# Kernel optimization log

Measured on AMD Instinct MI355X. Metric: run time of the kernel, lower is better.

The kernel has to match this reference:

```python
import jax, jax.numpy as jnp
import numpy as np

NODE_DIM = 128
EDGE_DIM = 128
N_RADIAL = 16
MAX_Z = 100
N_NODES = 50000
N_EDGES = 800000


def setup_inputs() -> dict:
    key = jax.random.key(0)
    ks = jax.random.split(key, 8)
    z = jax.random.randint(ks[0], (N_NODES,), 0, MAX_Z)
    rbf = jax.random.uniform(ks[1], (N_EDGES, N_RADIAL), dtype=jnp.float32)
    idx_i = jax.random.randint(ks[2], (N_EDGES,), 0, N_NODES)
    idx_j = jax.random.randint(ks[3], (N_EDGES,), 0, N_NODES)
    # learned parameters
    embed_table = jax.random.normal(ks[4], (MAX_Z, NODE_DIM), dtype=jnp.float32)
    rbf_w = jax.random.normal(ks[5], (N_RADIAL, EDGE_DIM), dtype=jnp.float32) * (1.0 / np.sqrt(N_RADIAL))
    in_dim = 2 * NODE_DIM + EDGE_DIM
    edge_w = jax.random.normal(ks[6], (in_dim, EDGE_DIM), dtype=jnp.float32) * (1.0 / np.sqrt(in_dim))
    edge_b = jnp.zeros((EDGE_DIM,), dtype=jnp.float32)
    return {"z": z, "rbf": rbf, "idx_i": idx_i, "idx_j": idx_j,
            "embed_table": embed_table, "rbf_w": rbf_w,
            "edge_w": edge_w, "edge_b": edge_b}


def reference(z, rbf, idx_i, idx_j, embed_table, rbf_w, edge_w, edge_b):
    # node embedding lookup: (n_node, node_dim)
    zemb = embed_table[z]
    # rbf projection (no bias): (n_edge, edge_dim)
    rbf_proj = rbf @ rbf_w
    # gather per-edge node embeddings and concat: (n_edge, 2*node_dim+edge_dim)
    feat = jnp.concatenate([zemb[idx_j], zemb[idx_i], rbf_proj], axis=-1)
    # Dense + swish
    h = feat @ edge_w + edge_b
    return h * jax.nn.sigmoid(h)
```

## Files before the change

### kernel.cpp

```cpp
#include <hip/hip_runtime.h>
#include <hip/hip_fp16.h>

#define NODE_DIM 128
#define EDGE_DIM 128
#define N_RADIAL 16
#define MAXZ     100
#define BLOCK    512
#define NWAVE    (BLOCK / 64)
#define MC       16

typedef _Float16 h2  __attribute__((ext_vector_type(2)));
typedef _Float16 h4  __attribute__((ext_vector_type(4)));
typedef float    fx4 __attribute__((ext_vector_type(4)));

__device__ __forceinline__ float fdot2f(h2 a, h2 b, float c) {
#if __has_builtin(__builtin_amdgcn_fdot2)
    return __builtin_amdgcn_fdot2(a, b, c, false);
#else
    return c + (float)a.x * (float)b.x + (float)a.y * (float)b.y;
#endif
}

__device__ __forceinline__ int pk16i(float x, float y) {
#if __has_builtin(__builtin_amdgcn_cvt_pkrtz)
    return __builtin_bit_cast(int, __builtin_amdgcn_cvt_pkrtz(x, y));
#else
    h2 v; v.x = (_Float16)x; v.y = (_Float16)y;
    return __builtin_bit_cast(int, v);
#endif
}

__global__ void precompute_all(const float* __restrict__ embed_table,
                               const float* __restrict__ edge_w,
                               const float* __restrict__ edge_b,
                               const float* __restrict__ rbf_w,
                               const int*   __restrict__ z,
                               const int*   __restrict__ idx_i,
                               const int*   __restrict__ idx_j,
                               __half* __restrict__ tH,
                               h2* __restrict__ w3h,
                               int* __restrict__ zpair,
                               int max_z, int n_edges, int do_zpair) {
    const int d = threadIdx.x;
    if ((int)blockIdx.x < max_z) {
        const int r = blockIdx.x;
        float s1 = edge_b[d];
        float s2 = 0.0f;
        const float* er = embed_table + (long)r * NODE_DIM;
#pragma unroll 8
        for (int k = 0; k < NODE_DIM; ++k) {
            const float e = er[k];
            s1 += e * edge_w[(long)k * EDGE_DIM + d];
            s2 += e * edge_w[(long)(NODE_DIM + k) * EDGE_DIM + d];
        }
        tH[(long)r * EDGE_DIM + d]          = __float2half(s1);
        tH[(long)(MAXZ + r) * EDGE_DIM + d] = __float2half(s2);
    } else if ((int)blockIdx.x < max_z + 8) {
        const int kk = blockIdx.x - max_z;
        const float* ra = rbf_w + (long)(2 * kk)     * EDGE_DIM;
        const float* rb = rbf_w + (long)(2 * kk + 1) * EDGE_DIM;
        float sa = 0.0f, sb = 0.0f;
#pragma unroll 8
        for (int k = 0; k < EDGE_DIM; ++k) {
            const float wkd = edge_w[(long)(2 * NODE_DIM + k) * EDGE_DIM + d];
            sa += ra[k] * wkd;
            sb += rb[k] * wkd;
        }
        h2 v; v.x = (_Float16)sa; v.y = (_Float16)sb;
        w3h[kk * EDGE_DIM + d] = v;
    } else if (do_zpair) {
        const int e = (blockIdx.x - (max_z + 8)) * EDGE_DIM + d;
        if (e < n_edges) {
            const int zj = z[idx_j[e]];
            const int zi = z[idx_i[e]];
            zpair[e] = (zj & 0xffff) | (zi << 16);
        }
    }
}

template <bool PRE>
__global__ void __launch_bounds__(BLOCK, 6) edge_main(
        const float* __restrict__ rbf,
        const int*   __restrict__ zpair,
        const int*   __restrict__ z,
        const int*   __restrict__ idx_i,
        const int*   __restrict__ idx_j,
        const h2*    __restrict__ tabg,
        const h2*    __restrict__ w3h,
        float* __restrict__ out,
        int n_edges) {
    __shared__ h2 sTab[2 * MAXZ * 64];

    const int tid  = threadIdx.x;
    const int lane = tid & 63;
    const int sub  = lane & 31;
    const int half = lane >> 5;

    h2 w[8][4];
#pragma unroll
    for (int kk = 0; kk < 8; ++kk) {
        const uint4 u = *reinterpret_cast<const uint4*>(
            &w3h[kk * EDGE_DIM + (sub << 2)]);
        w[kk][0] = __builtin_bit_cast(h2, u.x);
        w[kk][1] = __builtin_bit_cast(h2, u.y);
        w[kk][2] = __builtin_bit_cast(h2, u.z);
        w[kk][3] = __builtin_bit_cast(h2, u.w);
    }

    {
        const uint4* src = reinterpret_cast<const uint4*>(tabg);
        uint4*       dst = reinterpret_cast<uint4*>(sTab);
        for (int i = tid; i < (2 * MAXZ * EDGE_DIM) / 8; i += BLOCK)
            dst[i] = src[i];
    }
    __syncthreads();

    const int W   = gridDim.x * NWAVE;
    const int gw  = blockIdx.x * NWAVE + (tid >> 6);
    const int nmc = (n_edges + MC - 1) / MC;
    const int mlo = (int)(((long)gw * nmc) / W);
    const int mhi = (int)(((long)(gw + 1) * nmc) / W);
    if (mlo >= mhi) return;

    const fx4* rbf4 = reinterpret_cast<const fx4*>(rbf);
    const int  emax = n_edges - 1;
    const int  eoff = lane >> 2;
    const int  eqtr = lane & 3;
    const int  zoff = lane & 15;

#define GETZP(E) (PRE ? zpair[(E)] \
                      : ((z[idx_j[(E)]] & 0xffff) | (z[idx_i[(E)]] << 16)))
#define CLAMP(E) ((E) < emax ? (E) : emax)

    int rs0, rs1, zs;
    {
        const int e = CLAMP(mlo * MC + eoff);
        const fx4 v = rbf4[(long)e * 4 + eqtr];
        rs0 = pk16i(v.x, v.y);
        rs1 = pk16i(v.z, v.w);
        zs  = GETZP(CLAMP(mlo * MC + zoff));
    }

    for (int m = mlo; m < mhi; ++m) {
        const bool hasn = (m + 1) < mhi;

        fx4 nv = (fx4)0.0f;
        int nz = 0;
        if (hasn) {
            const int e = CLAMP((m + 1) * MC + eoff);
            nv = rbf4[(long)e * 4 + eqtr];
            nz = GETZP(CLAMP((m + 1) * MC + zoff));
        }

        const int base = m * MC;
#pragma unroll 2
        for (int s = 0; s < MC / 2; ++s) {
            const int el = (s << 1) | half;
            const int eg = base + el;

            const int zp = __shfl(zs, el);
            const int zj = zp & 0xffff;
            const int zi = zp >> 16;

            const h4 tj = *reinterpret_cast<const h4*>(
                &sTab[zj * 64 + (sub << 1)]);
            const h4 ti = *reinterpret_cast<const h4*>(
                &sTab[(MAXZ + zi) * 64 + (sub << 1)]);

            h2 rb[8];
#pragma unroll
            for (int t = 0; t < 8; ++t) {
                const int src = (el << 2) | (t >> 1);
                const int d   = __shfl((t & 1) ? rs1 : rs0, src);
                rb[t] = __builtin_bit_cast(h2, d);
            }

            const h4 t = tj + ti;
            float a0 = (float)t[0], a1 = (float)t[1];
            float a2 = (float)t[2], a3 = (float)t[3];

#pragma unroll
            for (int kk = 0; kk < 8; ++kk) {
                a0 = fdot2f(rb[kk], w[kk][0], a0);
                a1 = fdot2f(rb[kk], w[kk][1], a1);
                a2 = fdot2f(rb[kk], w[kk][2], a2);
                a3 = fdot2f(rb[kk], w[kk][3], a3);
            }

            fx4 o;
            o.x = a0 * __builtin_amdgcn_rcpf(1.0f + __expf(-a0));
            o.y = a1 * __builtin_amdgcn_rcpf(1.0f + __expf(-a1));
            o.z = a2 * __builtin_amdgcn_rcpf(1.0f + __expf(-a2));
            o.w = a3 * __builtin_amdgcn_rcpf(1.0f + __expf(-a3));

            if (eg <= emax)
                __builtin_nontemporal_store(o, reinterpret_cast<fx4*>(
                    &out[(size_t)eg * EDGE_DIM + (sub << 2)]));
        }

        if (hasn) {
            rs0 = pk16i(nv.x, nv.y);
            rs1 = pk16i(nv.z, nv.w);
            zs  = nz;
        }
    }
#undef GETZP
#undef CLAMP
}

extern "C" void kernel_launch(void* const* d_in, const int* in_sizes, int n_in,
                              void* d_out, int out_size, void* d_ws, size_t ws_size,
                              hipStream_t stream) {
    const int*   zp          = (const int*)  d_in[0];
    const float* rbf         = (const float*)d_in[1];
    const int*   idx_i       = (const int*)  d_in[2];
    const int*   idx_j       = (const int*)  d_in[3];
    const float* embed_table = (const float*)d_in[4];
    const float* rbf_w       = (const float*)d_in[5];
    const float* edge_w      = (const float*)d_in[6];
    const float* edge_b      = (const float*)d_in[7];

    int max_z = in_sizes[4] / NODE_DIM;
    if (max_z > MAXZ) max_z = MAXZ;
    const int n_edges = in_sizes[2];

    const size_t tab_bytes = (size_t)2 * MAXZ * EDGE_DIM * sizeof(__half);
    const size_t w3h_bytes = (size_t)8 * EDGE_DIM * sizeof(h2);
    __half* tH    = (__half*)d_ws;
    h2*     w3h   = (h2*)((char*)d_ws + tab_bytes);
    int*    zpair = (int*)((char*)d_ws + tab_bytes + w3h_bytes);
    const int use_zpair =
        (ws_size >= tab_bytes + w3h_bytes + (size_t)n_edges * sizeof(int)) ? 1 : 0;
    float* out = (float*)d_out;

    const int zblocks = use_zpair ? (n_edges + EDGE_DIM - 1) / EDGE_DIM : 0;
    precompute_all<<<max_z + 8 + zblocks, EDGE_DIM, 0, stream>>>(
        embed_table, edge_w, edge_b, rbf_w, zp, idx_i, idx_j,
        tH, w3h, zpair, max_z, n_edges, use_zpair);

    const int grid = 768;
    if (use_zpair)
        edge_main<true><<<grid, BLOCK, 0, stream>>>(rbf, zpair, zp, idx_i, idx_j,
                                                    (const h2*)tH, w3h, out, n_edges);
    else
        edge_main<false><<<grid, BLOCK, 0, stream>>>(rbf, zpair, zp, idx_i, idx_j,
                                                     (const h2*)tH, w3h, out, n_edges);
}
```

Measured before the change: 107.5 us.

## Remap edge work to one edge per wave with readlane broadcasts

Each wave now handles one edge at a time, with each of the 64 lanes computing two output channels, instead of two edges at once with 4 channels per lane. Per-edge node-type and rbf values are broadcast with readlane (scalar) instead of ds_bpermute shuffles, which removes LDS-routed shuffle traffic. The tradeoff is narrower 8-byte stores and table loads, fewer independent accumulators per lane, and a fully unrolled 16-step loop.

```diff
diff --git a/kernel.cpp b/kernel.cpp
--- a/kernel.cpp
+++ b/kernel.cpp
@@ -10,7 +10,7 @@
 #define MC       16
 
 typedef _Float16 h2  __attribute__((ext_vector_type(2)));
-typedef _Float16 h4  __attribute__((ext_vector_type(4)));
+typedef float    fx2 __attribute__((ext_vector_type(2)));
 typedef float    fx4 __attribute__((ext_vector_type(4)));
 
 __device__ __forceinline__ float fdot2f(h2 a, h2 b, float c) {
@@ -93,18 +93,14 @@
 
     const int tid  = threadIdx.x;
     const int lane = tid & 63;
-    const int sub  = lane & 31;
-    const int half = lane >> 5;
-
-    h2 w[8][4];
+
+    h2 w[8][2];
 #pragma unroll
     for (int kk = 0; kk < 8; ++kk) {
-        const uint4 u = *reinterpret_cast<const uint4*>(
-            &w3h[kk * EDGE_DIM + (sub << 2)]);
+        const uint2 u = *reinterpret_cast<const uint2*>(
+            &w3h[kk * EDGE_DIM + 2 * lane]);
         w[kk][0] = __builtin_bit_cast(h2, u.x);
         w[kk][1] = __builtin_bit_cast(h2, u.y);
-        w[kk][2] = __builtin_bit_cast(h2, u.z);
-        w[kk][3] = __builtin_bit_cast(h2, u.w);
     }
 
     {
@@ -153,49 +149,43 @@
         }
 
         const int base = m * MC;
-#pragma unroll 2
-        for (int s = 0; s < MC / 2; ++s) {
-            const int el = (s << 1) | half;
-            const int eg = base + el;
-
-            const int zp = __shfl(zs, el);
+#pragma unroll
+        for (int s = 0; s < MC; ++s) {
+            const int eg = base + s;
+
+            const int zp = __builtin_amdgcn_readlane(zs, s);
             const int zj = zp & 0xffff;
             const int zi = zp >> 16;
 
-            const h4 tj = *reinterpret_cast<const h4*>(
-                &sTab[zj * 64 + (sub << 1)]);
-            const h4 ti = *reinterpret_cast<const h4*>(
-                &sTab[(MAXZ + zi) * 64 + (sub << 1)]);
+            const h2 tj = sTab[zj * 64 + lane];
+            const h2 ti = sTab[(MAXZ + zi) * 64 + lane];
 
             h2 rb[8];
 #pragma unroll
             for (int t = 0; t < 8; ++t) {
-                const int src = (el << 2) | (t >> 1);
-                const int d   = __shfl((t & 1) ? rs1 : rs0, src);
+                const int src = (s << 2) | (t >> 1);
+                const int d   = __builtin_amdgcn_readlane((t & 1) ? rs1 : rs0,
+                                                          src);
                 rb[t] = __builtin_bit_cast(h2, d);
             }
 
-            const h4 t = tj + ti;
-            float a0 = (float)t[0], a1 = (float)t[1];
-            float a2 = (float)t[2], a3 = (float)t[3];
+            const h2 t = tj + ti;
+            float a0 = (float)t.x;
+            float a1 = (float)t.y;
 
 #pragma unroll
             for (int kk = 0; kk < 8; ++kk) {
                 a0 = fdot2f(rb[kk], w[kk][0], a0);
                 a1 = fdot2f(rb[kk], w[kk][1], a1);
-                a2 = fdot2f(rb[kk], w[kk][2], a2);
-                a3 = fdot2f(rb[kk], w[kk][3], a3);
             }
 
-            fx4 o;
+            fx2 o;
             o.x = a0 * __builtin_amdgcn_rcpf(1.0f + __expf(-a0));
             o.y = a1 * __builtin_amdgcn_rcpf(1.0f + __expf(-a1));
-            o.z = a2 * __builtin_amdgcn_rcpf(1.0f + __expf(-a2));
-            o.w = a3 * __builtin_amdgcn_rcpf(1.0f + __expf(-a3));
 
             if (eg <= emax)
-                __builtin_nontemporal_store(o, reinterpret_cast<fx4*>(
-                    &out[(size_t)eg * EDGE_DIM + (sub << 2)]));
+                __builtin_nontemporal_store(o, reinterpret_cast<fx2*>(
+                    &out[(size_t)eg * EDGE_DIM + 2 * lane]));
         }
 
         if (hasn) {
```

After: 106.5 us. No clear change (-0.9%).
